# Optimization experiments

Measured on AMD Instinct MI355X. Metric: run time of the kernel, lower is better.

The kernel has to match this reference:

```python
import jax, jax.numpy as jnp
import numpy as np

D_MODEL = 768
N_HEADS = 12
D_K = D_MODEL // N_HEADS
NEG_INF = -1e10


def setup_inputs() -> dict:
    key = jax.random.key(0)
    ks = jax.random.split(key, 12)
    B, S = 2, 4096
    scale = 1.0 / np.sqrt(D_MODEL)
    inp = {
        "q": jax.random.normal(ks[0], (B, S, D_MODEL), jnp.float32),
        "k": jax.random.normal(ks[1], (B, S, D_MODEL), jnp.float32),
        "v": jax.random.normal(ks[2], (B, S, D_MODEL), jnp.float32),
        "mask": jnp.ones((B, S), jnp.int32),
        "Wq": jax.random.normal(ks[3], (D_MODEL, D_MODEL), jnp.float32) * scale,
        "bq": jnp.zeros((D_MODEL,), jnp.float32),
        "Wk": jax.random.normal(ks[4], (D_MODEL, D_MODEL), jnp.float32) * scale,
        "bk": jnp.zeros((D_MODEL,), jnp.float32),
        "Wv": jax.random.normal(ks[5], (D_MODEL, D_MODEL), jnp.float32) * scale,
        "bv": jnp.zeros((D_MODEL,), jnp.float32),
        "Wo": jax.random.normal(ks[6], (D_MODEL, D_MODEL), jnp.float32) * scale,
        "bo": jnp.zeros((D_MODEL,), jnp.float32),
    }
    return inp


def reference(q, k, v, mask, Wq, bq, Wk, bk, Wv, bv, Wo, bo):
    B, Sq, _ = q.shape
    Sk = k.shape[1]
    # linear projections (flax Linear: x @ kernel + bias)
    query = q @ Wq + bq
    key_ = k @ Wk + bk
    value = v @ Wv + bv
    # split heads: [B, H, S, d_k]
    query = query.reshape(B, Sq, N_HEADS, D_K).transpose(0, 2, 1, 3)
    key_ = key_.reshape(B, Sk, N_HEADS, D_K).transpose(0, 2, 1, 3)
    value = value.reshape(B, Sk, N_HEADS, D_K).transpose(0, 2, 1, 3)
    # scores [B, H, Sq, Sk]
    scores = jnp.einsum('bhqd,bhkd->bhqk', query, key_) / jnp.sqrt(
        jnp.asarray(D_K, query.dtype))
    m = mask[:, None, None, :]  # 2D mask -> [B,1,1,Sk]
    scores = jnp.where(m == 0, NEG_INF, scores)
    attn = jax.nn.softmax(scores, axis=-1)
    # dropout deterministic (is_training=False): identity
    x = jnp.einsum('bhqk,bhkd->bhqd', attn, value)
    x = x.transpose(0, 2, 1, 3).reshape(B, Sq, D_MODEL)
    return x @ Wo + bo
```

## Files before the change

### kernel.cpp

```cpp
#include <hip/hip_runtime.h>

typedef __attribute__((ext_vector_type(8))) short short8;
typedef __attribute__((ext_vector_type(4))) float floatx4;
typedef __attribute__((ext_vector_type(16))) float floatx16;
typedef unsigned short ushort_t;

#define S_LEN 4096
#define NH 12
#define DK 64
#define DM 768
#define BQ 128
#define LOG2E 1.4426950408889634f

static __device__ __forceinline__ unsigned short f2bf(float f) {
    unsigned int u = __float_as_uint(f);
    u += 0x7FFFu + ((u >> 16) & 1u);
    return (unsigned short)(u >> 16);
}
static __device__ __forceinline__ unsigned pack2(float a, float b) {
    return (unsigned)f2bf(a) | ((unsigned)f2bf(b) << 16);
}
static __device__ __forceinline__ void gld_lds16(const void* g, void* l) {
    __builtin_amdgcn_global_load_lds(
        (__attribute__((address_space(1))) void*)g,
        (__attribute__((address_space(3))) void*)l, 16, 0, 0);
}

#define CVT_BLOCKS 9216
__global__ __launch_bounds__(256)
void prep_kernel(const float* __restrict__ A0, const float* __restrict__ A1,
                 const float* __restrict__ A2, ushort_t* __restrict__ O0,
                 ushort_t* __restrict__ O1, ushort_t* __restrict__ O2,
                 const float* __restrict__ W0, const float* __restrict__ W1,
                 const float* __restrict__ W2, const float* __restrict__ W3,
                 ushort_t* __restrict__ T0, ushort_t* __restrict__ T1,
                 ushort_t* __restrict__ T2, ushort_t* __restrict__ T3) {
    __shared__ float tile[32][33];
    const int gid = blockIdx.x;
    const int t = threadIdx.x;
    if (gid < CVT_BLOCKS) {
        const int z = gid / 3072;
        const int bidx = gid - z * 3072;
        const float* A = (z == 0) ? A0 : (z == 1) ? A1 : A2;
        ushort_t* O = (z == 0) ? O0 : (z == 1) ? O1 : O2;
        const size_t i = ((size_t)bidx * 256 + t) * 8;
        const float4 f0 = *(const float4*)(A + i);
        const float4 f1 = *(const float4*)(A + i + 4);
        uint4 o;
        o.x = pack2(f0.x, f0.y);
        o.y = pack2(f0.z, f0.w);
        o.z = pack2(f1.x, f1.y);
        o.w = pack2(f1.z, f1.w);
        *(uint4*)(O + i) = o;
    } else {
        const int gz = gid - CVT_BLOCKS;
        const int z = gz / 576;
        const int rem = gz - z * 576;
        const int bx = rem % 24, by = rem / 24;
        const float* W = (z == 0) ? W0 : (z == 1) ? W1 : (z == 2) ? W2 : W3;
        ushort_t* T = (z == 0) ? T0 : (z == 1) ? T1 : (z == 2) ? T2 : T3;
        const int tx = t & 31, ty = t >> 5;
        #pragma unroll
        for (int j = 0; j < 32; j += 8)
            tile[ty + j][tx] = W[(size_t)(by * 32 + ty + j) * DM + bx * 32 + tx];
        __syncthreads();
        #pragma unroll
        for (int j = 0; j < 32; j += 8)
            T[(size_t)(bx * 32 + ty + j) * DM + by * 32 + tx] = f2bf(tile[tx][ty + j]);
    }
}

struct GemmArgs {
    const ushort_t* A[3];
    const ushort_t* Wt[3];
    const float* bias[3];
    void* C[3];
    float scale[3];
};

template <int MODE>
__global__ __launch_bounds__(256, 3)
void gemm_kernel(GemmArgs args) {
    __shared__ __align__(16) ushort_t smem[128 * 136];
    ushort_t* As = smem;
    ushort_t* Bs = smem + 128 * 64;
    ushort_t* Ts = smem;
    const int z = blockIdx.z;
    const ushort_t* A = args.A[z];
    const ushort_t* Wt = args.Wt[z];
    const float* bias = args.bias[z];
    void* Carg = args.C[z];
    const float scale = args.scale[z];

    const int m0 = blockIdx.x * 128;
    const int n0 = blockIdx.y * 128;
    const int t = threadIdx.x;
    const int w = t >> 6, lane = t & 63, l15 = lane & 15, quad = lane >> 4;
    const int rowoff = (w >> 1) * 64, coloff = (w & 1) * 64;
    const int srow = w * 8 + (lane >> 3);
    const int schunk = lane & 7;
    const int gchunk = schunk ^ (lane >> 3);

    floatx4 acc[4][4];
    #pragma unroll
    for (int i = 0; i < 4; ++i)
        #pragma unroll
        for (int j = 0; j < 4; ++j) acc[i][j] = (floatx4){0.f, 0.f, 0.f, 0.f};

    for (int kt = 0; kt < DM; kt += 64) {
        __syncthreads();
        #pragma unroll
        for (int j = 0; j < 4; ++j) {
            const int r = j * 32 + srow;
            gld_lds16(A + (size_t)(m0 + r) * DM + kt + gchunk * 8,
                      &As[r * 64 + schunk * 8]);
        }
        #pragma unroll
        for (int j = 0; j < 4; ++j) {
            const int r = j * 32 + srow;
            gld_lds16(Wt + (size_t)(n0 + r) * DM + kt + gchunk * 8,
                      &Bs[r * 64 + schunk * 8]);
        }
        __asm__ __volatile__("s_waitcnt vmcnt(0)" ::: "memory");
        __syncthreads();

        #pragma unroll
        for (int kk = 0; kk < 2; ++kk) {
            short8 af[4], bfr[4];
            #pragma unroll
            for (int i = 0; i < 4; ++i) {
                const int r = rowoff + 16 * i + l15;
                af[i] = *(const short8*)&As[r * 64 + (((kk * 4 + quad) ^ (r & 7)) << 3)];
            }
            #pragma unroll
            for (int j = 0; j < 4; ++j) {
                const int r = coloff + 16 * j + l15;
                bfr[j] = *(const short8*)&Bs[r * 64 + (((kk * 4 + quad) ^ (r & 7)) << 3)];
            }
            #pragma unroll
            for (int i = 0; i < 4; ++i)
                #pragma unroll
                for (int j = 0; j < 4; ++j)
                    acc[i][j] = __builtin_amdgcn_mfma_f32_16x16x32_bf16(af[i], bfr[j], acc[i][j], 0, 0, 0);
        }
    }

    if (MODE == 0) {
        __syncthreads();
        if (z == 2) {
            #pragma unroll
            for (int i = 0; i < 4; ++i) {
                #pragma unroll
                for (int j = 0; j < 4; ++j) {
                    const int nl = coloff + 16 * j + l15;
                    const int mb = rowoff + 16 * i + quad * 4;
                    const float bn = bias[n0 + nl];
                    uint2 pk;
                    pk.x = pack2((acc[i][j][0] + bn) * scale, (acc[i][j][1] + bn) * scale);
                    pk.y = pack2((acc[i][j][2] + bn) * scale, (acc[i][j][3] + bn) * scale);
                    *(uint2*)&Ts[nl * 136 + mb] = pk;
                }
            }
            __syncthreads();
            ushort_t* VTout = (ushort_t*)Carg;
            #pragma unroll
            for (int pass = 0; pass < 8; ++pass) {
                const int row = pass * 16 + (t >> 4);
                const int c8 = (t & 15) * 8;
                const uint4 vv = *(const uint4*)&Ts[row * 136 + c8];
                const int n = n0 + row, h2 = n >> 6, d2 = n & 63;
                const int m = m0 + c8, b2 = m >> 12, s2 = m & 4095;
                *(uint4*)&VTout[((size_t)((b2 * NH + h2) * DK + d2)) * S_LEN + s2] = vv;
            }
        } else {
            #pragma unroll
            for (int i = 0; i < 4; ++i) {
                #pragma unroll
                for (int j = 0; j < 4; ++j) {
                    const int nl = coloff + 16 * j + l15;
                    const int mb = rowoff + 16 * i + quad * 4;
                    const float bn = bias[n0 + nl];
                    #pragma unroll
                    for (int reg = 0; reg < 4; ++reg)
                        Ts[(mb + reg) * 136 + nl] = f2bf((acc[i][j][reg] + bn) * scale);
                }
            }
            __syncthreads();
            ushort_t* Out = (ushort_t*)Carg;
            #pragma unroll
            for (int pass = 0; pass < 8; ++pass) {
                const int row = pass * 16 + (t >> 4);
                const int c8 = (t & 15) * 8;
                const uint4 vv = *(const uint4*)&Ts[row * 136 + c8];
                const int m = m0 + row, b2 = m >> 12, s2 = m & 4095;
                const int n = n0 + c8, h2 = n >> 6, d2 = n & 63;
                *(uint4*)&Out[((size_t)((b2 * NH + h2) * S_LEN + s2)) * DK + d2] = vv;
            }
        }
        return;
    }

    #pragma unroll
    for (int i = 0; i < 4; ++i) {
        #pragma unroll
        for (int j = 0; j < 4; ++j) {
            #pragma unroll
            for (int reg = 0; reg < 4; ++reg) {
                const int m = m0 + rowoff + 16 * i + quad * 4 + reg;
                const int n = n0 + coloff + 16 * j + l15;
                const float v2 = (acc[i][j][reg] + bias[n]) * scale;
                float* Out = (float*)Carg;
                Out[(size_t)m * DM + n] = v2;
            }
        }
    }
}

__global__ __launch_bounds__(256, 3)
void attn_kernel(const ushort_t* __restrict__ Q, const ushort_t* __restrict__ K,
                 const ushort_t* __restrict__ VT, const int* __restrict__ mask,
                 ushort_t* __restrict__ X) {
    __shared__ ushort_t Qs[BQ * DK];
    __shared__ ushort_t Ks0[64 * DK], Ks1[64 * DK];
    __shared__ ushort_t Vs0[64 * DK], Vs1[64 * DK];

    const int id = blockIdx.x;
    const int per = id >> 3;
    const int bh = (id & 7) * 3 + (per >> 5);
    const int qb = per & 31;
    const int b = bh / NH, h = bh - b * NH;
    const size_t bho = (size_t)bh * S_LEN;
    const ushort_t* Vbase = VT + (size_t)bh * DK * S_LEN;
    const int t = threadIdx.x;
    const int w = t >> 6, lane = t & 63, l31 = lane & 31, half = lane >> 5;
    const int q0 = qb * BQ;
    const int swl = l31 & 7;
    const int frow8 = lane >> 3;
    const int fcc = lane & 7;

    auto fillK = [&](int kv0, ushort_t* Kb) {
        #pragma unroll
        for (int j = 0; j < 2; ++j) {
            const int r = (w * 2 + j) * 8 + frow8;
            const int c8 = fcc ^ (r & 7);
            gld_lds16(K + (bho + kv0 + r) * DK + c8 * 8, &Kb[r * DK + fcc * 8]);
        }
    };
    auto fillV = [&](int kv0, ushort_t* Vb) {
        #pragma unroll
        for (int j = 0; j < 2; ++j) {
            const int r = (w * 2 + j) * 8 + frow8;
            const int c8 = fcc ^ (r & 7);
            gld_lds16(Vbase + (size_t)r * S_LEN + kv0 + c8 * 8, &Vb[r * DK + fcc * 8]);
        }
    };

    fillK(0, Ks0);
    fillV(0, Vs0);
    #pragma unroll
    for (int j = 0; j < 4; ++j) {
        const int r = (w * 4 + j) * 8 + frow8;
        const int c8 = fcc ^ (r & 7);
        gld_lds16(Q + (bho + q0 + r) * DK + c8 * 8, &Qs[r * DK + fcc * 8]);
    }
    int ok = 1;
    {
        const int* mrow = mask + (size_t)b * S_LEN + t * 16;
        #pragma unroll
        for (int i = 0; i < 4; ++i) {
            const int4 mm = *(const int4*)(mrow + i * 4);
            ok &= (mm.x != 0) & (mm.y != 0) & (mm.z != 0) & (mm.w != 0);
        }
    }
    const int allones = __syncthreads_and(ok);

    short8 qf[4];
    #pragma unroll
    for (int ks = 0; ks < 4; ++ks) {
        const int c8 = ks * 2 + half;
        qf[ks] = *(const short8*)&Qs[(w * 32 + l31) * DK + ((c8 ^ swl) << 3)];
    }

    floatx16 o[2];
    #pragma unroll
    for (int dt = 0; dt < 2; ++dt)
        #pragma unroll
        for (int r = 0; r < 16; ++r) o[dt][r] = 0.f;
    float l_r = 0.f;

    auto smt = [&](floatx16& stv, short8& plo, short8& phi) {
        float p[16];
        #pragma unroll
        for (int r = 0; r < 16; ++r) p[r] = __builtin_amdgcn_exp2f(stv[r]);
        #pragma unroll
        for (int g = 0; g < 4; ++g)
            l_r += (p[4 * g + 0] + p[4 * g + 1]) + (p[4 * g + 2] + p[4 * g + 3]);
        unsigned c0[4], c1[4];
        #pragma unroll
        for (int g = 0; g < 4; ++g) {
            asm("v_cvt_pk_bf16_f32 %0, %1, %2"
                : "=v"(c0[g]) : "v"(p[4 * g + 0]), "v"(p[4 * g + 1]));
            asm("v_cvt_pk_bf16_f32 %0, %1, %2"
                : "=v"(c1[g]) : "v"(p[4 * g + 2]), "v"(p[4 * g + 3]));
        }
        asm("v_permlane32_swap_b32 %0, %1" : "+v"(c0[0]), "+v"(c0[1]));
        asm("v_permlane32_swap_b32 %0, %1" : "+v"(c1[0]), "+v"(c1[1]));
        asm("v_permlane32_swap_b32 %0, %1" : "+v"(c0[2]), "+v"(c0[3]));
        asm("v_permlane32_swap_b32 %0, %1" : "+v"(c1[2]), "+v"(c1[3]));
        union { short8 s8; unsigned u[4]; } w0, w1;
        w0.u[0] = c0[0]; w0.u[1] = c1[0]; w0.u[2] = c0[1]; w0.u[3] = c1[1];
        w1.u[0] = c0[2]; w1.u[1] = c1[2]; w1.u[2] = c0[3]; w1.u[3] = c1[3];
        plo = w0.s8;
        phi = w1.s8;
    };

    auto body = [&](int it, const ushort_t* Kc, const ushort_t* Vc,
                    ushort_t* Kn, ushort_t* Vn) {
        __syncthreads();
        if (it + 1 < S_LEN / 64) {
            fillK((it + 1) * 64, Kn);
            fillV((it + 1) * 64, Vn);
        }
        unsigned long long mb = ~0ULL;
        if (!allones) {
            const int mv = mask[(size_t)b * S_LEN + it * 64 + lane];
            mb = __ballot(mv != 0);
        }

        floatx16 st[2];
        __builtin_amdgcn_s_setprio(1);
        #pragma unroll
        for (int kt = 0; kt < 2; ++kt) {
            floatx16 s;
            #pragma unroll
            for (int r = 0; r < 16; ++r) s[r] = 0.f;
            #pragma unroll
            for (int ks = 0; ks < 4; ++ks) {
                const int c8 = ks * 2 + half;
                const short8 kf = *(const short8*)&Kc[(kt * 32 + l31) * DK + ((c8 ^ swl) << 3)];
                s = __builtin_amdgcn_mfma_f32_32x32x16_bf16(kf, qf[ks], s, 0, 0, 0);
            }
            st[kt] = s;
        }
        __builtin_amdgcn_s_setprio(0);

        if (mb != ~0ULL) {
            #pragma unroll
            for (int kt = 0; kt < 2; ++kt) {
                const unsigned bits = (unsigned)(mb >> (kt * 32));
                const unsigned vbits = bits >> (half * 4);
                #pragma unroll
                for (int r = 0; r < 16; ++r)
                    if (!((vbits >> ((r & 3) + 8 * (r >> 2))) & 1)) st[kt][r] = -3.0e10f;
            }
        }

        short8 pf[4];
        smt(st[0], pf[0], pf[1]);
        __builtin_amdgcn_s_setprio(1);
        #pragma unroll
        for (int dt = 0; dt < 2; ++dt) {
            #pragma unroll
            for (int ks = 0; ks < 2; ++ks) {
                const int c8 = ks * 2 + half;
                const short8 vf = *(const short8*)&Vc[(dt * 32 + l31) * DK + ((c8 ^ swl) << 3)];
                o[dt] = __builtin_amdgcn_mfma_f32_32x32x16_bf16(pf[ks], vf, o[dt], 0, 0, 0);
            }
        }
        __builtin_amdgcn_s_setprio(0);
        smt(st[1], pf[2], pf[3]);
        __builtin_amdgcn_s_setprio(1);
        #pragma unroll
        for (int dt = 0; dt < 2; ++dt) {
            #pragma unroll
            for (int ks = 2; ks < 4; ++ks) {
                const int c8 = ks * 2 + half;
                const short8 vf = *(const short8*)&Vc[(dt * 32 + l31) * DK + ((c8 ^ swl) << 3)];
                o[dt] = __builtin_amdgcn_mfma_f32_32x32x16_bf16(pf[ks], vf, o[dt], 0, 0, 0);
            }
        }
        __builtin_amdgcn_s_setprio(0);
    };

    for (int it = 0; it < S_LEN / 64; it += 2) {
        body(it, Ks0, Vs0, Ks1, Vs1);
        body(it + 1, Ks1, Vs1, Ks0, Vs0);
    }

    l_r += __shfl_xor(l_r, 32);
    const float inv = 1.0f / l_r;
    float iv[16];
    #pragma unroll
    for (int r = 0; r < 16; ++r)
        iv[r] = __shfl(inv, (r & 3) + 8 * (r >> 2) + 4 * half);
    #pragma unroll
    for (int dt = 0; dt < 2; ++dt)
        #pragma unroll
        for (int r = 0; r < 16; ++r) {
            const int qrow = (r & 3) + 8 * (r >> 2) + 4 * half;
            const int s = q0 + w * 32 + qrow;
            const int d = h * DK + dt * 32 + l31;
            X[((size_t)b * S_LEN + s) * DM + d] = f2bf(o[dt][r] * iv[r]);
        }
}

extern "C" void kernel_launch(void* const* d_in, const int* in_sizes, int n_in,
                              void* d_out, int out_size, void* d_ws, size_t ws_size,
                              hipStream_t stream) {
    const float* q = (const float*)d_in[0];
    const float* k = (const float*)d_in[1];
    const float* v = (const float*)d_in[2];
    const int* mask = (const int*)d_in[3];
    const float* Wq = (const float*)d_in[4];
    const float* bq = (const float*)d_in[5];
    const float* Wk = (const float*)d_in[6];
    const float* bk = (const float*)d_in[7];
    const float* Wv = (const float*)d_in[8];
    const float* bv = (const float*)d_in[9];
    const float* Wo = (const float*)d_in[10];
    const float* bo = (const float*)d_in[11];
    float* out = (float*)d_out;

    const size_t ME = (size_t)2 * S_LEN * DM;
    const size_t WE = (size_t)DM * DM;
    ushort_t* Qb = (ushort_t*)d_ws;
    ushort_t* Kb = Qb + ME;
    ushort_t* Vb = Kb + ME;
    ushort_t* VTb = Vb + ME;
    ushort_t* Xb = VTb + ME;
    ushort_t* Wqt = Xb + ME;
    ushort_t* Wkt = Wqt + WE;
    ushort_t* Wvt = Wkt + WE;
    ushort_t* Wot = Wvt + WE;
    ushort_t* Qa = Xb;
    ushort_t* Ka = Vb;
    ushort_t* Va = (ushort_t*)d_out;

    prep_kernel<<<dim3(CVT_BLOCKS + 2304), 256, 0, stream>>>(
        q, k, v, Qa, Ka, Va, Wq, Wk, Wv, Wo, Wqt, Wkt, Wvt, Wot);

    GemmArgs g1;
    g1.A[0] = Qa;  g1.A[1] = Ka;  g1.A[2] = Va;
    g1.Wt[0] = Wqt; g1.Wt[1] = Wkt; g1.Wt[2] = Wvt;
    g1.bias[0] = bq; g1.bias[1] = bk; g1.bias[2] = bv;
    g1.C[0] = Qb;  g1.C[1] = Kb;  g1.C[2] = VTb;
    g1.scale[0] = 0.125f * LOG2E;
    g1.scale[1] = 1.0f; g1.scale[2] = 1.0f;
    gemm_kernel<0><<<dim3((2 * S_LEN) / 128, DM / 128, 3), 256, 0, stream>>>(g1);

    attn_kernel<<<dim3(768), 256, 0, stream>>>(Qb, Kb, VTb, mask, Xb);

    GemmArgs g2;
    g2.A[0] = Xb;  g2.A[1] = Xb;  g2.A[2] = Xb;
    g2.Wt[0] = Wot; g2.Wt[1] = Wot; g2.Wt[2] = Wot;
    g2.bias[0] = bo; g2.bias[1] = bo; g2.bias[2] = bo;
    g2.C[0] = out; g2.C[1] = out; g2.C[2] = out;
    g2.scale[0] = 1.0f; g2.scale[1] = 1.0f; g2.scale[2] = 1.0f;
    gemm_kernel<1><<<dim3((2 * S_LEN) / 128, DM / 128, 1), 256, 0, stream>>>(g2);
}
```

Measured before the change: 315.2 us.

## Split attention over two KV halves with a combine kernel

The attention kernel now splits each query block's key/value range into two halves, so the grid doubles to 1536 blocks. Each half writes partial normalized outputs and row sums, and a new combine kernel merges them using the row-sum weights. This works without a running max because the scores are not max-subtracted. LDS is trimmed by dropping the Q tile and single-buffering V, and the launch-bounds occupancy hint rises to 6, with extra barriers and vmcnt waits per iteration. The aim is better CU utilization and occupancy, paid for by an extra kernel launch, extra memory traffic for the partials, and a less overlapped V load.

```diff
diff --git a/kernel.cpp b/kernel.cpp
--- a/kernel.cpp
+++ b/kernel.cpp
@@ -216,18 +216,19 @@
     }
 }
 
-__global__ __launch_bounds__(256, 3)
+__global__ __launch_bounds__(256, 6)
 void attn_kernel(const ushort_t* __restrict__ Q, const ushort_t* __restrict__ K,
                  const ushort_t* __restrict__ VT, const int* __restrict__ mask,
-                 ushort_t* __restrict__ X) {
-    __shared__ ushort_t Qs[BQ * DK];
-    __shared__ ushort_t Ks0[64 * DK], Ks1[64 * DK];
-    __shared__ ushort_t Vs0[64 * DK], Vs1[64 * DK];
+                 ushort_t* __restrict__ O0p, ushort_t* __restrict__ O1p,
+                 float* __restrict__ Lp) {
+    __shared__ ushort_t Ks0[64 * DK], Ks1[64 * DK], Vs[64 * DK];
 
     const int id = blockIdx.x;
     const int per = id >> 3;
-    const int bh = (id & 7) * 3 + (per >> 5);
-    const int qb = per & 31;
+    const int bh = (id & 7) * 3 + per / 64;
+    const int rem = per % 64;
+    const int qb = rem >> 1;
+    const int kvh = rem & 1;
     const int b = bh / NH, h = bh - b * NH;
     const size_t bho = (size_t)bh * S_LEN;
     const ushort_t* Vbase = VT + (size_t)bh * DK * S_LEN;
@@ -237,6 +238,9 @@
     const int swl = l31 & 7;
     const int frow8 = lane >> 3;
     const int fcc = lane & 7;
+    const int g0 = kvh * 32;
+    ushort_t* Op = kvh ? O1p : O0p;
+    float* Lrow = Lp + (size_t)(kvh * 24 + bh) * S_LEN;
 
     auto fillK = [&](int kv0, ushort_t* Kb) {
         #pragma unroll
@@ -246,23 +250,20 @@
             gld_lds16(K + (bho + kv0 + r) * DK + c8 * 8, &Kb[r * DK + fcc * 8]);
         }
     };
-    auto fillV = [&](int kv0, ushort_t* Vb) {
+    auto fillV = [&](int kv0) {
         #pragma unroll
         for (int j = 0; j < 2; ++j) {
             const int r = (w * 2 + j) * 8 + frow8;
             const int c8 = fcc ^ (r & 7);
-            gld_lds16(Vbase + (size_t)r * S_LEN + kv0 + c8 * 8, &Vb[r * DK + fcc * 8]);
+            gld_lds16(Vbase + (size_t)r * S_LEN + kv0 + c8 * 8, &Vs[r * DK + fcc * 8]);
         }
     };
 
-    fillK(0, Ks0);
-    fillV(0, Vs0);
-    #pragma unroll
-    for (int j = 0; j < 4; ++j) {
-        const int r = (w * 4 + j) * 8 + frow8;
-        const int c8 = fcc ^ (r & 7);
-        gld_lds16(Q + (bho + q0 + r) * DK + c8 * 8, &Qs[r * DK + fcc * 8]);
-    }
+    fillK(g0 * 64, Ks0);
+    short8 qf[4];
+    #pragma unroll
+    for (int ks = 0; ks < 4; ++ks)
+        qf[ks] = *(const short8*)&Q[(bho + q0 + w * 32 + l31) * DK + ks * 16 + half * 8];
     int ok = 1;
     {
         const int* mrow = mask + (size_t)b * S_LEN + t * 16;
@@ -273,13 +274,6 @@
         }
     }
     const int allones = __syncthreads_and(ok);
-
-    short8 qf[4];
-    #pragma unroll
-    for (int ks = 0; ks < 4; ++ks) {
-        const int c8 = ks * 2 + half;
-        qf[ks] = *(const short8*)&Qs[(w * 32 + l31) * DK + ((c8 ^ swl) << 3)];
-    }
 
     floatx16 o[2];
     #pragma unroll
@@ -314,16 +308,15 @@
         phi = w1.s8;
     };
 
-    auto body = [&](int it, const ushort_t* Kc, const ushort_t* Vc,
-                    ushort_t* Kn, ushort_t* Vn) {
-        __syncthreads();
-        if (it + 1 < S_LEN / 64) {
-            fillK((it + 1) * 64, Kn);
-            fillV((it + 1) * 64, Vn);
-        }
+    for (int it = 0; it < 32; ++it) {
+        const int g = g0 + it;
+        const ushort_t* Kc = (it & 1) ? Ks1 : Ks0;
+        ushort_t* Kn = (it & 1) ? Ks0 : Ks1;
+        fillV(g * 64);
+        if (it + 1 < 32) fillK((g + 1) * 64, Kn);
         unsigned long long mb = ~0ULL;
         if (!allones) {
-            const int mv = mask[(size_t)b * S_LEN + it * 64 + lane];
+            const int mv = mask[(size_t)b * S_LEN + g * 64 + lane];
             mb = __ballot(mv != 0);
         }
 
@@ -357,38 +350,28 @@
 
         short8 pf[4];
         smt(st[0], pf[0], pf[1]);
+        smt(st[1], pf[2], pf[3]);
+
+        __asm__ __volatile__("s_waitcnt vmcnt(0)" ::: "memory");
+        __syncthreads();
+
         __builtin_amdgcn_s_setprio(1);
         #pragma unroll
         for (int dt = 0; dt < 2; ++dt) {
             #pragma unroll
-            for (int ks = 0; ks < 2; ++ks) {
+            for (int ks = 0; ks < 4; ++ks) {
                 const int c8 = ks * 2 + half;
-                const short8 vf = *(const short8*)&Vc[(dt * 32 + l31) * DK + ((c8 ^ swl) << 3)];
+                const short8 vf = *(const short8*)&Vs[(dt * 32 + l31) * DK + ((c8 ^ swl) << 3)];
                 o[dt] = __builtin_amdgcn_mfma_f32_32x32x16_bf16(pf[ks], vf, o[dt], 0, 0, 0);
             }
         }
         __builtin_amdgcn_s_setprio(0);
-        smt(st[1], pf[2], pf[3]);
-        __builtin_amdgcn_s_setprio(1);
-        #pragma unroll
-        for (int dt = 0; dt < 2; ++dt) {
-            #pragma unroll
-            for (int ks = 2; ks < 4; ++ks) {
-                const int c8 = ks * 2 + half;
-                const short8 vf = *(const short8*)&Vc[(dt * 32 + l31) * DK + ((c8 ^ swl) << 3)];
-                o[dt] = __builtin_amdgcn_mfma_f32_32x32x16_bf16(pf[ks], vf, o[dt], 0, 0, 0);
-            }
-        }
-        __builtin_amdgcn_s_setprio(0);
-    };
-
-    for (int it = 0; it < S_LEN / 64; it += 2) {
-        body(it, Ks0, Vs0, Ks1, Vs1);
-        body(it + 1, Ks1, Vs1, Ks0, Vs0);
+        __syncthreads();
     }
 
     l_r += __shfl_xor(l_r, 32);
-    const float inv = 1.0f / l_r;
+    if (half == 0) Lrow[q0 + w * 32 + l31] = l_r;
+    const float inv = (l_r > 0.f) ? (1.0f / l_r) : 0.f;
     float iv[16];
     #pragma unroll
     for (int r = 0; r < 16; ++r)
@@ -400,8 +383,39 @@
             const int qrow = (r & 3) + 8 * (r >> 2) + 4 * half;
             const int s = q0 + w * 32 + qrow;
             const int d = h * DK + dt * 32 + l31;
-            X[((size_t)b * S_LEN + s) * DM + d] = f2bf(o[dt][r] * iv[r]);
-        }
+            Op[((size_t)b * S_LEN + s) * DM + d] = f2bf(o[dt][r] * iv[r]);
+        }
+}
+
+__global__ __launch_bounds__(256)
+void combine_kernel(const ushort_t* __restrict__ O0, const ushort_t* __restrict__ O1,
+                    const float* __restrict__ Lp, ushort_t* __restrict__ X) {
+    const size_t idx = ((size_t)blockIdx.x * 256 + threadIdx.x) * 8;
+    const int d = (int)(idx % DM);
+    const size_t bs = idx / DM;
+    const int s = (int)(bs % S_LEN);
+    const int b = (int)(bs / S_LEN);
+    const int bh = b * NH + (d >> 6);
+    const float l0 = Lp[(size_t)bh * S_LEN + s];
+    const float l1 = Lp[(size_t)(24 + bh) * S_LEN + s];
+    const float ls = l0 + l1;
+    const float r = (ls > 0.f) ? (1.0f / ls) : 0.f;
+    const float w0 = l0 * r, w1 = l1 * r;
+    const uint4 a = *(const uint4*)(O0 + idx);
+    const uint4 c = *(const uint4*)(O1 + idx);
+    auto comb2 = [&](unsigned ua, unsigned uc) -> unsigned {
+        const float a0 = __uint_as_float(ua << 16);
+        const float a1 = __uint_as_float(ua & 0xFFFF0000u);
+        const float c0 = __uint_as_float(uc << 16);
+        const float c1 = __uint_as_float(uc & 0xFFFF0000u);
+        return pack2(w0 * a0 + w1 * c0, w0 * a1 + w1 * c1);
+    };
+    uint4 o;
+    o.x = comb2(a.x, c.x);
+    o.y = comb2(a.y, c.y);
+    o.z = comb2(a.z, c.z);
+    o.w = comb2(a.w, c.w);
+    *(uint4*)(X + idx) = o;
 }
 
 extern "C" void kernel_launch(void* const* d_in, const int* in_sizes, int n_in,
@@ -435,6 +449,9 @@
     ushort_t* Qa = Xb;
     ushort_t* Ka = Vb;
     ushort_t* Va = (ushort_t*)d_out;
+    ushort_t* Op0 = Vb;
+    ushort_t* Op1 = (ushort_t*)d_out;
+    float* Lp = (float*)((ushort_t*)d_out + ME);
 
     prep_kernel<<<dim3(CVT_BLOCKS + 2304), 256, 0, stream>>>(
         q, k, v, Qa, Ka, Va, Wq, Wk, Wv, Wo, Wqt, Wkt, Wvt, Wot);
@@ -448,7 +465,9 @@
     g1.scale[1] = 1.0f; g1.scale[2] = 1.0f;
     gemm_kernel<0><<<dim3((2 * S_LEN) / 128, DM / 128, 3), 256, 0, stream>>>(g1);
 
-    attn_kernel<<<dim3(768), 256, 0, stream>>>(Qb, Kb, VTb, mask, Xb);
+    attn_kernel<<<dim3(1536), 256, 0, stream>>>(Qb, Kb, VTb, mask, Op0, Op1, Lp);
+
+    combine_kernel<<<dim3((int)(ME / 8 / 256)), 256, 0, stream>>>(Op0, Op1, Lp, Xb);
 
     GemmArgs g2;
     g2.A[0] = Xb;  g2.A[1] = Xb;  g2.A[2] = Xb;
```

Result: slower. 791.5 us (+151.1%).
